# Kernel tuning notes

Hardware: AMD Instinct MI355X
Metric: run time of the kernel (lower is better)

Reference implementation:

```python
import jax, jax.numpy as jnp
import numpy as np

EMBED_D = 128
NUM_NODES = 10000
NUM_EDGE_TYPES = 14
BATCH = 8192
EDGE_IN = EMBED_D * 12   # 1536
HET_IN = EMBED_D * 14    # 1792


def setup_inputs() -> dict:
    key = jax.random.key(0)
    ks = jax.random.split(key, 6)
    features = jax.random.normal(ks[0], (NUM_EDGE_TYPES, NUM_NODES, EDGE_IN), dtype=jnp.float32)
    W_edge = jax.random.normal(ks[1], (NUM_EDGE_TYPES, EDGE_IN, EMBED_D), dtype=jnp.float32) * 0.02
    b_edge = jnp.full((NUM_EDGE_TYPES, EMBED_D), 0.1, dtype=jnp.float32)
    W_het = jax.random.normal(ks[2], (HET_IN, EMBED_D), dtype=jnp.float32) * 0.02
    b_het = jnp.full((EMBED_D,), 0.1, dtype=jnp.float32)
    gid_batch = jax.random.randint(ks[3], (BATCH,), 0, NUM_NODES, dtype=jnp.int64 if jax.config.read('jax_enable_x64') else jnp.int32)
    return {"features": features, "W_edge": W_edge, "b_edge": b_edge,
            "W_het": W_het, "b_het": b_het, "gid_batch": gid_batch}


def reference(features, W_edge, b_edge, W_het, b_het, gid_batch):
    # Gather per edge type: [E, B, embed_d*12]
    gathered = features[:, gid_batch]
    # 14 parallel linear + LeakyReLU (torch default slope 0.01)
    h = jnp.einsum('ebd,edk->ebk', gathered, W_edge) + b_edge[:, None, :]  # [E, B, embed_d]
    h = jax.nn.leaky_relu(h, 0.01)
    # concat along feature dim in edge-type order: [B, 14*embed_d]
    agg = jnp.transpose(h, (1, 0, 2)).reshape(gid_batch.shape[0], -1)
    out = jax.nn.leaky_relu(agg @ W_het + b_het, 0.01)  # [B, embed_d]
    return out
```

## Files before the change

kernel.cpp:

```cpp
#include <hip/hip_runtime.h>
#include <hip/hip_bf16.h>
#include <stdint.h>

#define NE 14
#define NN 10000
#define ED 128
#define KE 1536
#define KH 1792
#define NB 8192

typedef __attribute__((ext_vector_type(4))) float f32x4;
typedef __attribute__((ext_vector_type(8))) short s16x8;

__device__ __forceinline__ short f2bf(float f) {
  union { float f; uint32_t u; } v; v.f = f;
  uint32_t r = (v.u + 0x7fffu + ((v.u >> 16) & 1u)) >> 16;
  return (short)r;
}

__global__ __launch_bounds__(256) void prep_transpose(
    const float* __restrict__ We, const float* __restrict__ Wh,
    short* __restrict__ WtE, short* __restrict__ WtH) {
  __shared__ float tile[64][65];
  int b = blockIdx.x;
  int t = threadIdx.x;
  const float* src; short* dst; int K; int kt, nt;
  if (b < NE * 48) {
    int e = b / 48; int r = b % 48;
    kt = r >> 1; nt = r & 1;
    src = We + (size_t)e * KE * ED;
    dst = WtE + (size_t)e * ED * KE;
    K = KE;
  } else {
    int r = b - NE * 48;
    kt = r >> 1; nt = r & 1;
    src = Wh; dst = WtH; K = KH;
  }
  int k0 = kt * 64, n0 = nt * 64;
  for (int i = 0; i < 16; i++) {
    int idx = i * 256 + t;
    int kk = idx >> 6, nn = idx & 63;
    tile[kk][nn] = src[(size_t)(k0 + kk) * ED + n0 + nn];
  }
  __syncthreads();
  for (int i = 0; i < 16; i++) {
    int idx = i * 256 + t;
    int nn = idx >> 6, kk = idx & 63;
    dst[(size_t)(n0 + nn) * K + k0 + kk] = f2bf(tile[kk][nn]);
  }
}

__global__ __launch_bounds__(256) void stage1(
    const float* __restrict__ feat, const short* __restrict__ WtE,
    const float* __restrict__ b_edge, const int* __restrict__ gid,
    short* __restrict__ agg) {
  __shared__ short Alds[128 * 64];
  __shared__ short Blds[128 * 64];
  int t = threadIdx.x;
  int e = blockIdx.y;
  int m0 = blockIdx.x * 128;

  int rowA = t >> 3;
  int cA = t & 7;
  const float* baseA[4];
  for (int i = 0; i < 4; i++) {
    int g = gid[m0 + rowA + 32 * i];
    baseA[i] = feat + ((size_t)e * NN + (size_t)g) * KE;
  }
  const short* baseB = WtE + (size_t)e * ED * KE;

  int lane = t & 63;
  int wave = t >> 6;
  int wm = wave >> 1, wn = wave & 1;
  int quad = lane >> 4, l16 = lane & 15;

  f32x4 zero = {0.f, 0.f, 0.f, 0.f};
  f32x4 acc[4][4];
  for (int i = 0; i < 4; i++) for (int j = 0; j < 4; j++) acc[i][j] = zero;

  for (int k0 = 0; k0 < KE; k0 += 64) {
    for (int i = 0; i < 4; i++) {
      const float* p = baseA[i] + k0 + cA * 8;
      f32x4 x0 = *(const f32x4*)p;
      f32x4 x1 = *(const f32x4*)(p + 4);
      s16x8 v;
      v[0] = f2bf(x0[0]); v[1] = f2bf(x0[1]); v[2] = f2bf(x0[2]); v[3] = f2bf(x0[3]);
      v[4] = f2bf(x1[0]); v[5] = f2bf(x1[1]); v[6] = f2bf(x1[2]); v[7] = f2bf(x1[3]);
      int m = rowA + 32 * i;
      *(s16x8*)&Alds[m * 64 + ((cA ^ (m & 7)) << 3)] = v;
    }
    for (int i = 0; i < 4; i++) {
      int n = rowA + 32 * i;
      s16x8 v = *(const s16x8*)(baseB + (size_t)n * KE + k0 + cA * 8);
      *(s16x8*)&Blds[n * 64 + ((cA ^ (n & 7)) << 3)] = v;
    }
    __syncthreads();
    for (int ks = 0; ks < 2; ks++) {
      s16x8 af[4], bfr[4];
      for (int mt = 0; mt < 4; mt++) {
        int m = wm * 64 + mt * 16 + l16;
        af[mt] = *(const s16x8*)&Alds[m * 64 + (((ks * 4 + quad) ^ (m & 7)) << 3)];
      }
      for (int nt = 0; nt < 4; nt++) {
        int n = wn * 64 + nt * 16 + l16;
        bfr[nt] = *(const s16x8*)&Blds[n * 64 + (((ks * 4 + quad) ^ (n & 7)) << 3)];
      }
      for (int mt = 0; mt < 4; mt++)
        for (int nt = 0; nt < 4; nt++)
          acc[mt][nt] = __builtin_amdgcn_mfma_f32_16x16x32_bf16(af[mt], bfr[nt], acc[mt][nt], 0, 0, 0);
    }
    __syncthreads();
  }

  float bias[4];
  for (int nt = 0; nt < 4; nt++) bias[nt] = b_edge[e * ED + wn * 64 + nt * 16 + l16];
  for (int mt = 0; mt < 4; mt++) {
    int mg = m0 + wm * 64 + mt * 16 + quad * 4;
    for (int nt = 0; nt < 4; nt++) {
      int ng = e * ED + wn * 64 + nt * 16 + l16;
      for (int r = 0; r < 4; r++) {
        float v = acc[mt][nt][r] + bias[nt];
        v = v > 0.f ? v : 0.01f * v;
        agg[(size_t)(mg + r) * KH + ng] = f2bf(v);
      }
    }
  }
}

__global__ __launch_bounds__(256) void stage2(
    const short* __restrict__ agg, const short* __restrict__ WtH,
    const float* __restrict__ b_het, float* __restrict__ out) {
  __shared__ short Alds[32 * 64];
  __shared__ short Blds[128 * 64];
  int t = threadIdx.x;
  int m0 = blockIdx.x * 32;
  int rowA = t >> 3, cA = t & 7;
  int lane = t & 63, wave = t >> 6;
  int wm = wave & 1, wn = wave >> 1;
  int quad = lane >> 4, l16 = lane & 15;

  f32x4 zero = {0.f, 0.f, 0.f, 0.f};
  f32x4 acc[4];
  for (int i = 0; i < 4; i++) acc[i] = zero;

  for (int k0 = 0; k0 < KH; k0 += 64) {
    {
      s16x8 v = *(const s16x8*)(agg + (size_t)(m0 + rowA) * KH + k0 + cA * 8);
      *(s16x8*)&Alds[rowA * 64 + ((cA ^ (rowA & 7)) << 3)] = v;
    }
    for (int i = 0; i < 4; i++) {
      int n = rowA + 32 * i;
      s16x8 v = *(const s16x8*)(WtH + (size_t)n * KH + k0 + cA * 8);
      *(s16x8*)&Blds[n * 64 + ((cA ^ (n & 7)) << 3)] = v;
    }
    __syncthreads();
    for (int ks = 0; ks < 2; ks++) {
      int m = wm * 16 + l16;
      s16x8 a = *(const s16x8*)&Alds[m * 64 + (((ks * 4 + quad) ^ (m & 7)) << 3)];
      for (int nt = 0; nt < 4; nt++) {
        int n = wn * 64 + nt * 16 + l16;
        s16x8 b = *(const s16x8*)&Blds[n * 64 + (((ks * 4 + quad) ^ (n & 7)) << 3)];
        acc[nt] = __builtin_amdgcn_mfma_f32_16x16x32_bf16(a, b, acc[nt], 0, 0, 0);
      }
    }
    __syncthreads();
  }

  for (int nt = 0; nt < 4; nt++) {
    int ng = wn * 64 + nt * 16 + l16;
    float bias = b_het[ng];
    for (int r = 0; r < 4; r++) {
      float v = acc[nt][r] + bias;
      v = v > 0.f ? v : 0.01f * v;
      out[(size_t)(m0 + wm * 16 + quad * 4 + r) * ED + ng] = v;
    }
  }
}

extern "C" void kernel_launch(void* const* d_in, const int* in_sizes, int n_in,
                              void* d_out, int out_size, void* d_ws, size_t ws_size,
                              hipStream_t stream) {
  const float* feat = (const float*)d_in[0];
  const float* We   = (const float*)d_in[1];
  const float* be   = (const float*)d_in[2];
  const float* Wh   = (const float*)d_in[3];
  const float* bh   = (const float*)d_in[4];
  const int*   gid  = (const int*)d_in[5];
  float* out = (float*)d_out;

  char* ws = (char*)d_ws;
  short* WtE = (short*)ws;
  short* WtH = (short*)(ws + 5505024);
  short* agg = (short*)(ws + 5505024 + 458752);

  prep_transpose<<<NE * 48 + 56, 256, 0, stream>>>(We, Wh, WtE, WtH);
  dim3 g1(NB / 128, NE);
  stage1<<<g1, 256, 0, stream>>>(feat, WtE, be, gid, agg);
  stage2<<<NB / 32, 256, 0, stream>>>(agg, WtH, bh, out);
}
```

Before: 1.075 ms.

## Double-buffer stage1 GEMM with async global-to-LDS weight loads and 512 threads

Stage1 now uses 512 threads per block with a K-step of 32 and double-buffered LDS tiles. Weight tiles go straight from global memory to LDS through the global_load_lds builtin, and the next feature rows are prefetched into registers while MFMAs run on the current buffer. This is meant to hide the latency of the gathered feature loads behind compute, at the cost of twice as many K iterations and barriers and a smaller per-wave tile. The B tile loses its XOR swizzle, which may cause LDS bank conflicts.

```diff
diff --git a/kernel.cpp b/kernel.cpp
--- a/kernel.cpp
+++ b/kernel.cpp
@@ -50,72 +50,85 @@
   }
 }
 
-__global__ __launch_bounds__(256) void stage1(
+__global__ __launch_bounds__(512) void stage1(
     const float* __restrict__ feat, const short* __restrict__ WtE,
     const float* __restrict__ b_edge, const int* __restrict__ gid,
     short* __restrict__ agg) {
-  __shared__ short Alds[128 * 64];
-  __shared__ short Blds[128 * 64];
+  __shared__ short Alds[2][128 * 32];
+  __shared__ short Blds[2][128 * 32];
   int t = threadIdx.x;
   int e = blockIdx.y;
   int m0 = blockIdx.x * 128;
 
-  int rowA = t >> 3;
-  int cA = t & 7;
-  const float* baseA[4];
-  for (int i = 0; i < 4; i++) {
-    int g = gid[m0 + rowA + 32 * i];
-    baseA[i] = feat + ((size_t)e * NN + (size_t)g) * KE;
-  }
-  const short* baseB = WtE + (size_t)e * ED * KE;
-
-  int lane = t & 63;
-  int wave = t >> 6;
+  int rowA = t >> 2, cA = t & 3;
+  const float* rowp = feat + ((size_t)e * NN + (size_t)gid[m0 + rowA]) * KE;
+
+  int bn = t >> 2, bk = t & 3;
+  const short* bsrc = WtE + (size_t)e * ED * KE + (size_t)bn * KE + bk * 8;
+
+  int wave = t >> 6, lane = t & 63;
+  int quad = lane >> 4, l16 = lane & 15;
   int wm = wave >> 1, wn = wave & 1;
-  int quad = lane >> 4, l16 = lane & 15;
 
   f32x4 zero = {0.f, 0.f, 0.f, 0.f};
-  f32x4 acc[4][4];
-  for (int i = 0; i < 4; i++) for (int j = 0; j < 4; j++) acc[i][j] = zero;
-
-  for (int k0 = 0; k0 < KE; k0 += 64) {
-    for (int i = 0; i < 4; i++) {
-      const float* p = baseA[i] + k0 + cA * 8;
-      f32x4 x0 = *(const f32x4*)p;
-      f32x4 x1 = *(const f32x4*)(p + 4);
+  f32x4 acc[2][4];
+  for (int i = 0; i < 2; i++) for (int j = 0; j < 4; j++) acc[i][j] = zero;
+
+  {
+    short* bl = &Blds[0][0] + (size_t)wave * 512;
+    __builtin_amdgcn_global_load_lds(
+        (const __attribute__((address_space(1))) void*)(bsrc),
+        (__attribute__((address_space(3))) void*)bl, 16, 0, 0);
+    f32x4 x0 = *(const f32x4*)(rowp + cA * 8);
+    f32x4 x1 = *(const f32x4*)(rowp + cA * 8 + 4);
+    s16x8 v;
+    v[0] = f2bf(x0[0]); v[1] = f2bf(x0[1]); v[2] = f2bf(x0[2]); v[3] = f2bf(x0[3]);
+    v[4] = f2bf(x1[0]); v[5] = f2bf(x1[1]); v[6] = f2bf(x1[2]); v[7] = f2bf(x1[3]);
+    *(s16x8*)&Alds[0][rowA * 32 + ((cA ^ (rowA & 3)) << 3)] = v;
+  }
+  __syncthreads();
+
+  for (int kt = 0; kt < KE / 32; kt++) {
+    int cur = kt & 1;
+    int nxt = cur ^ 1;
+    bool hn = (kt + 1) < KE / 32;
+    f32x4 x0, x1;
+    if (hn) {
+      int k1 = (kt + 1) * 32;
+      x0 = *(const f32x4*)(rowp + k1 + cA * 8);
+      x1 = *(const f32x4*)(rowp + k1 + cA * 8 + 4);
+      short* bl = &Blds[nxt][0] + (size_t)wave * 512;
+      __builtin_amdgcn_global_load_lds(
+          (const __attribute__((address_space(1))) void*)(bsrc + k1),
+          (__attribute__((address_space(3))) void*)bl, 16, 0, 0);
+    }
+    {
+      s16x8 af[2], bfr[4];
+      for (int mt = 0; mt < 2; mt++) {
+        int m = wm * 32 + mt * 16 + l16;
+        af[mt] = *(const s16x8*)&Alds[cur][m * 32 + ((quad ^ (m & 3)) << 3)];
+      }
+      for (int nt = 0; nt < 4; nt++) {
+        int n = wn * 64 + nt * 16 + l16;
+        bfr[nt] = *(const s16x8*)&Blds[cur][n * 32 + quad * 8];
+      }
+      for (int mt = 0; mt < 2; mt++)
+        for (int nt = 0; nt < 4; nt++)
+          acc[mt][nt] = __builtin_amdgcn_mfma_f32_16x16x32_bf16(af[mt], bfr[nt], acc[mt][nt], 0, 0, 0);
+    }
+    if (hn) {
       s16x8 v;
       v[0] = f2bf(x0[0]); v[1] = f2bf(x0[1]); v[2] = f2bf(x0[2]); v[3] = f2bf(x0[3]);
       v[4] = f2bf(x1[0]); v[5] = f2bf(x1[1]); v[6] = f2bf(x1[2]); v[7] = f2bf(x1[3]);
-      int m = rowA + 32 * i;
-      *(s16x8*)&Alds[m * 64 + ((cA ^ (m & 7)) << 3)] = v;
-    }
-    for (int i = 0; i < 4; i++) {
-      int n = rowA + 32 * i;
-      s16x8 v = *(const s16x8*)(baseB + (size_t)n * KE + k0 + cA * 8);
-      *(s16x8*)&Blds[n * 64 + ((cA ^ (n & 7)) << 3)] = v;
-    }
-    __syncthreads();
-    for (int ks = 0; ks < 2; ks++) {
-      s16x8 af[4], bfr[4];
-      for (int mt = 0; mt < 4; mt++) {
-        int m = wm * 64 + mt * 16 + l16;
-        af[mt] = *(const s16x8*)&Alds[m * 64 + (((ks * 4 + quad) ^ (m & 7)) << 3)];
-      }
-      for (int nt = 0; nt < 4; nt++) {
-        int n = wn * 64 + nt * 16 + l16;
-        bfr[nt] = *(const s16x8*)&Blds[n * 64 + (((ks * 4 + quad) ^ (n & 7)) << 3)];
-      }
-      for (int mt = 0; mt < 4; mt++)
-        for (int nt = 0; nt < 4; nt++)
-          acc[mt][nt] = __builtin_amdgcn_mfma_f32_16x16x32_bf16(af[mt], bfr[nt], acc[mt][nt], 0, 0, 0);
+      *(s16x8*)&Alds[nxt][rowA * 32 + ((cA ^ (rowA & 3)) << 3)] = v;
     }
     __syncthreads();
   }
 
   float bias[4];
   for (int nt = 0; nt < 4; nt++) bias[nt] = b_edge[e * ED + wn * 64 + nt * 16 + l16];
-  for (int mt = 0; mt < 4; mt++) {
-    int mg = m0 + wm * 64 + mt * 16 + quad * 4;
+  for (int mt = 0; mt < 2; mt++) {
+    int mg = m0 + wm * 32 + mt * 16 + quad * 4;
     for (int nt = 0; nt < 4; nt++) {
       int ng = e * ED + wn * 64 + nt * 16 + l16;
       for (int r = 0; r < 4; r++) {
@@ -195,6 +208,6 @@
 
   prep_transpose<<<NE * 48 + 56, 256, 0, stream>>>(We, Wh, WtE, WtH);
   dim3 g1(NB / 128, NE);
-  stage1<<<g1, 256, 0, stream>>>(feat, WtE, be, gid, agg);
+  stage1<<<g1, 512, 0, stream>>>(feat, WtE, be, gid, agg);
   stage2<<<NB / 32, 256, 0, stream>>>(agg, WtH, bh, out);
 }
```

Result: slower. 1.103 ms (+2.7%).
